# Optimization experiments

Hardware: AMD Instinct MI355X
Metric: run time of the kernel (lower is better)

The kernel has to match this reference:

```python
import jax, jax.numpy as jnp
import numpy as np

HEAD_DIM = 128
MAX_TIMESCALE = 10000.0
MIN_TIMESCALE = 1.0


def _rope(x, pos):
    # x: [B, S, H, D], pos: [B, S]
    d = x.shape[-1]
    fraction = 2.0 * jnp.arange(0, d // 2, dtype=jnp.float32) / d
    timescale = MIN_TIMESCALE * (MAX_TIMESCALE / MIN_TIMESCALE) ** fraction  # [D/2]
    sinusoid = pos.astype(jnp.float32)[..., None, None] / timescale  # [B,S,1,D/2]
    sin, cos = jnp.sin(sinusoid), jnp.cos(sinusoid)
    xf = x.astype(jnp.float32)
    x1, x2 = jnp.split(xf, 2, axis=-1)
    return jnp.concatenate((x1 * cos - x2 * sin, x2 * cos + x1 * sin), axis=-1).astype(x.dtype)


def setup_inputs() -> dict:
    key = jax.random.key(0)
    ks = jax.random.split(key, 5)
    B, T, D, N, K, H = 2, 2048, 2048, 16, 4, HEAD_DIM
    s = 0.02
    X = jax.random.normal(ks[0], (B, T, D), dtype=jnp.float32)
    q_positions = jnp.broadcast_to(jnp.arange(T, dtype=jnp.int32), (B, T))
    Wq = jax.random.normal(ks[1], (D, N, H), dtype=jnp.float32) * s
    Wk = jax.random.normal(ks[2], (D, K, H), dtype=jnp.float32) * s
    Wv = jax.random.normal(ks[3], (D, K, H), dtype=jnp.float32) * s
    Wo = jax.random.normal(ks[4], (N, H, D), dtype=jnp.float32) * s
    return {"X": X, "q_positions": q_positions, "Wq": Wq, "Wk": Wk, "Wv": Wv, "Wo": Wo}


def reference(X, q_positions, Wq, Wk, Wv, Wo):
    B, T, D = X.shape
    N, K = Wq.shape[1], Wk.shape[1]
    groups = N // K
    # fused QKV projections (DenseGeneral, no bias)
    q = jnp.einsum('btd,dnh->btnh', X, Wq)  # [B,T,N,H]
    k = jnp.einsum('btd,dkh->btkh', X, Wk)  # [B,T,K,H]
    v = jnp.einsum('btd,dkh->btkh', X, Wv)  # [B,T,K,H]
    # RoPE (note: original uses q_positions sin/cos for both q and k in the no-cache path)
    q = _rope(q, q_positions)
    k = _rope(k, q_positions)
    # GQA: broadcast kv heads to query heads
    k = jnp.repeat(k, groups, axis=2)  # [B,T,N,H]
    v = jnp.repeat(v, groups, axis=2)
    # attention with scale=1.0 and causal masking
    scores = jnp.einsum('btnh,bsnh->bnts', q, k)  # [B,N,T,T]
    causal = jnp.tril(jnp.ones((T, T), dtype=bool))
    scores = jnp.where(causal, scores, jnp.finfo(scores.dtype).min)
    probs = jax.nn.softmax(scores, axis=-1)
    attn = jnp.einsum('bnts,bsnh->btnh', probs, v)  # [B,T,N,H]
    # output projection contracting (head, head_dim)
    out = jnp.einsum('btnh,nhd->btd', attn, Wo)
    return out.astype(X.dtype)
```

## Files before the change

### kernel.cpp

```cpp
#include <hip/hip_runtime.h>
#include <math.h>

#define DEVI static __device__ __forceinline__

using f16x8 = __attribute__((ext_vector_type(8))) _Float16;
using h16x2 = __attribute__((ext_vector_type(2))) __fp16;
using f32x4  = __attribute__((ext_vector_type(4))) float;

constexpr int Bb = 2, Tt = 2048, Dd = 2048, NQ = 16, NK = 4, HD = 128;
constexpr int Mrows = Bb * Tt;
constexpr int QKVC  = NQ*HD + 2*NK*HD;
constexpr int KOFF  = NQ*HD;
constexpr int VOFF  = NQ*HD + NK*HD;

DEVI ushort f2h(float f) {
  _Float16 h = (_Float16)f;
  union { _Float16 h; ushort u; } v; v.h = h;
  return v.u;
}
DEVI float h2f(ushort u) {
  union { ushort u; _Float16 h; } v; v.u = u;
  return (float)v.h;
}

typedef const __attribute__((address_space(1))) unsigned* gp1;
typedef __attribute__((address_space(3))) unsigned* lp3;
DEVI void gload16(void* lds, const void* g) {
  __builtin_amdgcn_global_load_lds((gp1)g, (lp3)lds, 16, 0, 0);
}

__global__ void k_cvt(const float* __restrict__ x, ushort* __restrict__ o, int n4) {
  int i = blockIdx.x * blockDim.x + threadIdx.x;
  if (i >= n4) return;
  float4 v = ((const float4*)x)[i];
  ushort4 u;
  u.x = f2h(v.x); u.y = f2h(v.y); u.z = f2h(v.z); u.w = f2h(v.w);
  ((ushort4*)o)[i] = u;
}

__global__ void k_tconv(const float* __restrict__ in, ushort* __restrict__ out, int R, int C) {
  __shared__ float t[32][33];
  const int c0 = blockIdx.x * 32, r0 = blockIdx.y * 32;
  const int tx = threadIdx.x, ty = threadIdx.y;
#pragma unroll
  for (int i = 0; i < 32; i += 8)
    t[ty + i][tx] = in[(size_t)(r0 + ty + i) * C + (c0 + tx)];
  __syncthreads();
#pragma unroll
  for (int i = 0; i < 32; i += 8)
    out[(size_t)(c0 + ty + i) * R + (r0 + tx)] = f2h(t[tx][ty + i]);
}

DEVI void stv(float* p, float v)  { *p = v; }
DEVI void stv(ushort* p, float v) { *p = f2h(v); }

template <typename OT>
__launch_bounds__(256)
__global__ void k_gemm_bt(const ushort* __restrict__ A, const ushort* __restrict__ Bt,
                          OT* __restrict__ C, int M, int N, int Kd) {
  __shared__ char As[8192];
  __shared__ char Bs[8192];
  const int tid = threadIdx.x;
  const int l = tid & 63, w = tid >> 6;
  const int wr = w >> 1, wc = w & 1;
  const int lr = l & 15, lk = l >> 4;
  const size_t row0 = (size_t)blockIdx.y * 128, col0 = (size_t)blockIdx.x * 128;

  f32x4 acc[4][4];
#pragma unroll
  for (int i = 0; i < 4; ++i)
#pragma unroll
    for (int j = 0; j < 4; ++j) acc[i][j] = (f32x4){0.f, 0.f, 0.f, 0.f};

  const int c0i = tid, c1i = tid + 256;
  const int ra0 = c0i >> 2, sa0 = (c0i & 3) ^ ((ra0 >> 1) & 3);
  const int ra1 = c1i >> 2, sa1 = (c1i & 3) ^ ((ra1 >> 1) & 3);

  for (int kt = 0; kt < Kd; kt += 32) {
    if (kt) __syncthreads();
    gload16(As + c0i * 16, A + (row0 + ra0) * Kd + kt + sa0 * 8);
    gload16(As + c1i * 16, A + (row0 + ra1) * Kd + kt + sa1 * 8);
    gload16(Bs + c0i * 16, Bt + (col0 + ra0) * Kd + kt + sa0 * 8);
    gload16(Bs + c1i * 16, Bt + (col0 + ra1) * Kd + kt + sa1 * 8);
    __syncthreads();
    f16x8 af[4], bfr[4];
#pragma unroll
    for (int i = 0; i < 4; ++i) {
      int ra = wr * 64 + i * 16 + lr;
      af[i] = *(const f16x8*)(As + ra * 64 + ((lk ^ ((ra >> 1) & 3)) << 4));
      int rb = wc * 64 + i * 16 + lr;
      bfr[i] = *(const f16x8*)(Bs + rb * 64 + ((lk ^ ((rb >> 1) & 3)) << 4));
    }
#pragma unroll
    for (int i = 0; i < 4; ++i)
#pragma unroll
      for (int j = 0; j < 4; ++j)
        acc[i][j] = __builtin_amdgcn_mfma_f32_16x16x32_f16(af[i], bfr[j], acc[i][j], 0, 0, 0);
  }
#pragma unroll
  for (int i = 0; i < 4; ++i) {
    size_t r = row0 + wr * 64 + i * 16 + lk * 4;
#pragma unroll
    for (int j = 0; j < 4; ++j) {
      size_t cc = col0 + wc * 64 + j * 16 + lr;
#pragma unroll
      for (int rg = 0; rg < 4; ++rg) stv(&C[(r + rg) * N + cc], acc[i][j][rg]);
    }
  }
}

__global__ void k_rope_tab(const int* __restrict__ pos, float* __restrict__ tab) {
  int idx = blockIdx.x * blockDim.x + threadIdx.x;
  if (idx >= Mrows * 64) return;
  int m = idx >> 6, i = idx & 63;
  double a = (double)pos[m] * exp2(-0.20762050593045952 * (double)i);
  tab[idx * 2]     = (float)cos(a);
  tab[idx * 2 + 1] = (float)sin(a);
}

__global__ void k_rope(ushort* __restrict__ qkv, const float* __restrict__ tab) {
  int idx = blockIdx.x * blockDim.x + threadIdx.x;
  if (idx >= Mrows * 20 * 8) return;
  int chunk = idx & 7;
  int h20 = (idx >> 3) % 20;
  int m = idx / 160;
  int colbase = (h20 < 16) ? h20 * 128 : (KOFF + (h20 - 16) * 128);
  size_t base = (size_t)m * QKVC + colbase + chunk * 8;
  union { uint4 v; ushort s[8]; } A1, A2, O1, O2;
  A1.v = *(const uint4*)(qkv + base);
  A2.v = *(const uint4*)(qkv + base + 64);
  const float* tp = tab + ((size_t)m * 64 + chunk * 8) * 2;
#pragma unroll
  for (int j = 0; j < 8; ++j) {
    float c = tp[2 * j], s = tp[2 * j + 1];
    float x1 = h2f(A1.s[j]), x2 = h2f(A2.s[j]);
    O1.s[j] = f2h(x1 * c - x2 * s);
    O2.s[j] = f2h(x2 * c + x1 * s);
  }
  *(uint4*)(qkv + base) = O1.v;
  *(uint4*)(qkv + base + 64) = O2.v;
}

__global__ void k_vt(const ushort* __restrict__ qkv, ushort* __restrict__ vt) {
  __shared__ ushort t[32][33];
  const int bg = blockIdx.z, bq = bg >> 2, g = bg & 3;
  const int s0 = blockIdx.x * 32, h0 = blockIdx.y * 32;
  const int tx = threadIdx.x, ty = threadIdx.y;
#pragma unroll
  for (int i = 0; i < 32; i += 8)
    t[ty + i][tx] = qkv[(size_t)(bq * Tt + s0 + ty + i) * QKVC + VOFF + g * HD + h0 + tx];
  __syncthreads();
#pragma unroll
  for (int i = 0; i < 32; i += 8)
    vt[((size_t)bg * HD + h0 + ty + i) * Tt + (s0 + tx)] = t[tx][ty + i];
}

__launch_bounds__(512, 2)
__global__ void k_flash(const ushort* __restrict__ qkv, const ushort* __restrict__ vt,
                        ushort* __restrict__ attn) {
  __shared__ char Ks[2][16384];
  __shared__ char Vs[2][16384];
  __shared__ char Pl[8][2048];
  const int b = blockIdx.x;
  const int vv = b >> 8, u = b & 255;
  const int hid = u >> 3, p = u & 7;
  const int qt = vv ? p : (15 - p);
  const int bq = hid >> 4, n = hid & 15, g = n >> 2;
  const int tid = threadIdx.x, w = tid >> 6, l = tid & 63;
  const int lr = l & 15, lk = l >> 4;
  const int t0 = qt * 128;
  const int qrow = t0 + w * 16;
  const int qglob = qrow + lr;

  f16x8 qf[4];
  {
    const size_t qb = ((size_t)(bq * Tt + qrow + lr)) * QKVC + n * HD + lk * 8;
#pragma unroll
    for (int kt = 0; kt < 4; ++kt) qf[kt] = *(const f16x8*)(qkv + qb + kt * 32);
  }
  f32x4 O[8];
#pragma unroll
  for (int hb = 0; hb < 8; ++hb) O[hb] = (f32x4){0.f, 0.f, 0.f, 0.f};
  float m = -INFINITY, lsum = 0.f;

  const size_t kgbase = (size_t)(bq * Tt) * QKVC + KOFF + g * HD;
  const size_t vgbase = (size_t)(bq * 4 + g) * HD * Tt;
  const int ntiles = 2 * qt + 2;

  int srow[2], koin[2], hrow[2], voin[2];
#pragma unroll
  for (int cc = 0; cc < 2; ++cc) {
    int c = cc * 512 + tid;
    srow[cc] = c >> 4;
    koin[cc] = (((c & 15) << 4) ^ ((srow[cc] & 7) << 4)) >> 1;
    hrow[cc] = c >> 3;
    voin[cc] = (((c & 7) << 4) ^ ((hrow[cc] & 7) << 4)) >> 1;
  }

#define STAGE(buf, s0s)                                                              \
  {                                                                                  \
    _Pragma("unroll")                                                                \
    for (int cc = 0; cc < 2; ++cc) {                                                 \
      int c16 = (cc * 512 + tid) * 16;                                               \
      gload16(Ks[buf] + c16, qkv + kgbase + (size_t)((s0s) + srow[cc]) * QKVC + koin[cc]); \
      gload16(Vs[buf] + c16, vt + vgbase + (size_t)hrow[cc] * Tt + (s0s) + voin[cc]); \
    }                                                                                \
  }

  STAGE(0, 0);
  __syncthreads();

  for (int j = 0; j < ntiles; ++j) {
    const int cur = j & 1;
    if (j + 1 < ntiles) STAGE(cur ^ 1, (j + 1) * 64);
    const int s0 = j * 64;
    if (s0 <= qrow + 15) {
      f32x4 sc[4];
      __builtin_amdgcn_s_setprio(1);
#pragma unroll
      for (int ns = 0; ns < 4; ++ns) {
        f32x4 a = (f32x4){0.f, 0.f, 0.f, 0.f};
        int sl = ns * 16 + lr;
#pragma unroll
        for (int kt = 0; kt < 4; ++kt) {
          int inner = (kt * 64 + lk * 16) ^ ((sl & 7) << 4);
          f16x8 kf = *(const f16x8*)(Ks[cur] + sl * 256 + inner);
          a = __builtin_amdgcn_mfma_f32_16x16x32_f16(kf, qf[kt], a, 0, 0, 0);
        }
        sc[ns] = a;
      }
      __builtin_amdgcn_s_setprio(0);
      if (s0 + 63 > qrow) {
#pragma unroll
        for (int ns = 0; ns < 4; ++ns)
#pragma unroll
          for (int r = 0; r < 4; ++r)
            if (s0 + ns * 16 + lk * 4 + r > qglob) sc[ns][r] = -INFINITY;
      }
      float pm = -INFINITY;
#pragma unroll
      for (int ns = 0; ns < 4; ++ns)
        pm = fmaxf(pm, fmaxf(fmaxf(sc[ns][0], sc[ns][1]), fmaxf(sc[ns][2], sc[ns][3])));
      pm = fmaxf(pm, __shfl_xor(pm, 16));
      pm = fmaxf(pm, __shfl_xor(pm, 32));
      const bool doresc = !__all(pm - m <= 8.0f);
      float scl = 1.f;
      if (doresc) { float mn = fmaxf(m, pm); scl = __expf(m - mn); m = mn; }
      float rs = 0.f;
#pragma unroll
      for (int ns = 0; ns < 4; ++ns) {
#pragma unroll
        for (int r = 0; r < 4; ++r) sc[ns][r] = __expf(sc[ns][r] - m);
        rs += (sc[ns][0] + sc[ns][1]) + (sc[ns][2] + sc[ns][3]);
      }
      rs += __shfl_xor(rs, 16);
      rs += __shfl_xor(rs, 32);
      char* pwb = Pl[w] + lr * 128;
      const int swz = (lr & 7) << 4;
#pragma unroll
      for (int ns = 0; ns < 4; ++ns) {
        union { h16x2 h[2]; uint2 u; } pk;
        pk.h[0] = __builtin_amdgcn_cvt_pkrtz(sc[ns][0], sc[ns][1]);
        pk.h[1] = __builtin_amdgcn_cvt_pkrtz(sc[ns][2], sc[ns][3]);
        *(uint2*)(pwb + ((ns * 32 + lk * 8) ^ swz)) = pk.u;
      }
      if (doresc) {
        float sr[4];
#pragma unroll
        for (int r = 0; r < 4; ++r) sr[r] = __shfl(scl, lk * 4 + r);
#pragma unroll
        for (int hb = 0; hb < 8; ++hb)
#pragma unroll
          for (int r = 0; r < 4; ++r) O[hb][r] *= sr[r];
        lsum = lsum * scl + rs;
      } else {
        lsum += rs;
      }
      f16x8 pa0 = *(const f16x8*)(pwb + ((lk * 16) ^ swz));
      f16x8 pa1 = *(const f16x8*)(pwb + ((64 + lk * 16) ^ swz));
      __builtin_amdgcn_s_setprio(1);
#pragma unroll
      for (int hb = 0; hb < 8; ++hb) {
        int h = hb * 16 + lr;
        int inner0 = (lk * 16) ^ ((h & 7) << 4);
        f16x8 vf0 = *(const f16x8*)(Vs[cur] + h * 128 + inner0);
        O[hb] = __builtin_amdgcn_mfma_f32_16x16x32_f16(pa0, vf0, O[hb], 0, 0, 0);
        int inner1 = (64 + lk * 16) ^ ((h & 7) << 4);
        f16x8 vf1 = *(const f16x8*)(Vs[cur] + h * 128 + inner1);
        O[hb] = __builtin_amdgcn_mfma_f32_16x16x32_f16(pa1, vf1, O[hb], 0, 0, 0);
      }
      __builtin_amdgcn_s_setprio(0);
    }
    __syncthreads();
  }
#undef STAGE
  float iv[4];
#pragma unroll
  for (int r = 0; r < 4; ++r) iv[r] = 1.f / __shfl(lsum, lk * 4 + r);
#pragma unroll
  for (int hb = 0; hb < 8; ++hb)
#pragma unroll
    for (int r = 0; r < 4; ++r) {
      size_t orow = (size_t)(bq * Tt + qrow + lk * 4 + r);
      attn[orow * 2048 + n * HD + hb * 16 + lr] = f2h(O[hb][r] * iv[r]);
    }
}

extern "C" void kernel_launch(void* const* d_in, const int* in_sizes, int n_in,
                              void* d_out, int out_size, void* d_ws, size_t ws_size,
                              hipStream_t stream) {
  const float* X  = (const float*)d_in[0];
  const int*   qp = (const int*)d_in[1];
  const float* Wq = (const float*)d_in[2];
  const float* Wk = (const float*)d_in[3];
  const float* Wv = (const float*)d_in[4];
  const float* Wo = (const float*)d_in[5];
  float* out = (float*)d_out;
  char* ws = (char*)d_ws;

  ushort* Xf    = (ushort*)(ws + 0);
  ushort* WqkvT = (ushort*)(ws + 16777216);
  ushort* WoT   = (ushort*)(ws + 29360128);
  ushort* QKV   = (ushort*)(ws + 37748736);
  ushort* VT    = (ushort*)(ws + 62914560);
  ushort* attn  = (ushort*)(ws + 67108864);
  float*  tab   = (float*)(ws + 83886080);

  dim3 tb(32, 8);
  k_cvt<<<(Mrows * Dd / 4 + 255) / 256, 256, 0, stream>>>(X, Xf, Mrows * Dd / 4);
  k_tconv<<<dim3(64, 64), tb, 0, stream>>>(Wq, WqkvT, Dd, NQ * HD);
  k_tconv<<<dim3(16, 64), tb, 0, stream>>>(Wk, WqkvT + (size_t)KOFF * Dd, Dd, NK * HD);
  k_tconv<<<dim3(16, 64), tb, 0, stream>>>(Wv, WqkvT + (size_t)VOFF * Dd, Dd, NK * HD);
  k_tconv<<<dim3(64, 64), tb, 0, stream>>>(Wo, WoT, NQ * HD, Dd);
  k_gemm_bt<ushort><<<dim3(QKVC / 128, Mrows / 128), 256, 0, stream>>>(
      Xf, WqkvT, QKV, Mrows, QKVC, Dd);
  k_rope_tab<<<(Mrows * 64 + 255) / 256, 256, 0, stream>>>(qp, tab);
  k_rope<<<(Mrows * 160 + 255) / 256, 256, 0, stream>>>(QKV, tab);
  k_vt<<<dim3(Tt / 32, HD / 32, Bb * NK), tb, 0, stream>>>(QKV, VT);
  k_flash<<<dim3(512), 512, 0, stream>>>(QKV, VT, attn);
  k_gemm_bt<float><<<dim3(Dd / 128, Mrows / 128), 256, 0, stream>>>(
      attn, WoT, out, Mrows, Dd, Dd);
}
```

Measured before the change: 216.8 us.

## Switch flash attention to 32x32x16 MFMA with register-resident P and 4 waves

```diff
diff --git a/kernel.cpp b/kernel.cpp
--- a/kernel.cpp
+++ b/kernel.cpp
@@ -6,6 +6,7 @@
 using f16x8 = __attribute__((ext_vector_type(8))) _Float16;
 using h16x2 = __attribute__((ext_vector_type(2))) __fp16;
 using f32x4  = __attribute__((ext_vector_type(4))) float;
+using f32x16 = __attribute__((ext_vector_type(16))) float;
 
 constexpr int Bb = 2, Tt = 2048, Dd = 2048, NQ = 16, NK = 4, HD = 128;
 constexpr int Mrows = Bb * Tt;
@@ -150,61 +151,55 @@
   for (int i = 0; i < 32; i += 8)
     t[ty + i][tx] = qkv[(size_t)(bq * Tt + s0 + ty + i) * QKVC + VOFF + g * HD + h0 + tx];
   __syncthreads();
+  const int sx = (tx & 3) | ((tx & 8) >> 1) | ((tx & 4) << 1) | (tx & 16);
 #pragma unroll
   for (int i = 0; i < 32; i += 8)
-    vt[((size_t)bg * HD + h0 + ty + i) * Tt + (s0 + tx)] = t[tx][ty + i];
-}
-
-__launch_bounds__(512, 2)
+    vt[((size_t)bg * HD + h0 + ty + i) * Tt + (s0 + sx)] = t[tx][ty + i];
+}
+
+__launch_bounds__(256, 2)
 __global__ void k_flash(const ushort* __restrict__ qkv, const ushort* __restrict__ vt,
                         ushort* __restrict__ attn) {
   __shared__ char Ks[2][16384];
   __shared__ char Vs[2][16384];
-  __shared__ char Pl[8][2048];
   const int b = blockIdx.x;
   const int vv = b >> 8, u = b & 255;
   const int hid = u >> 3, p = u & 7;
   const int qt = vv ? p : (15 - p);
   const int bq = hid >> 4, n = hid & 15, g = n >> 2;
   const int tid = threadIdx.x, w = tid >> 6, l = tid & 63;
-  const int lr = l & 15, lk = l >> 4;
+  const int q5 = l & 31, hi = l >> 5;
   const int t0 = qt * 128;
-  const int qrow = t0 + w * 16;
-  const int qglob = qrow + lr;
-
-  f16x8 qf[4];
+  const int qrow = t0 + w * 32;
+  const int qglob = qrow + q5;
+
+  f16x8 qf[8];
   {
-    const size_t qb = ((size_t)(bq * Tt + qrow + lr)) * QKVC + n * HD + lk * 8;
-#pragma unroll
-    for (int kt = 0; kt < 4; ++kt) qf[kt] = *(const f16x8*)(qkv + qb + kt * 32);
-  }
-  f32x4 O[8];
-#pragma unroll
-  for (int hb = 0; hb < 8; ++hb) O[hb] = (f32x4){0.f, 0.f, 0.f, 0.f};
+    const size_t qb = ((size_t)(bq * Tt + qglob)) * QKVC + n * HD + hi * 8;
+#pragma unroll
+    for (int kc = 0; kc < 8; ++kc) qf[kc] = *(const f16x8*)(qkv + qb + kc * 16);
+  }
+  f32x16 O[4];
+#pragma unroll
+  for (int ht = 0; ht < 4; ++ht)
+#pragma unroll
+    for (int r = 0; r < 16; ++r) O[ht][r] = 0.f;
   float m = -INFINITY, lsum = 0.f;
 
   const size_t kgbase = (size_t)(bq * Tt) * QKVC + KOFF + g * HD;
   const size_t vgbase = (size_t)(bq * 4 + g) * HD * Tt;
   const int ntiles = 2 * qt + 2;
 
-  int srow[2], koin[2], hrow[2], voin[2];
-#pragma unroll
-  for (int cc = 0; cc < 2; ++cc) {
-    int c = cc * 512 + tid;
-    srow[cc] = c >> 4;
-    koin[cc] = (((c & 15) << 4) ^ ((srow[cc] & 7) << 4)) >> 1;
-    hrow[cc] = c >> 3;
-    voin[cc] = (((c & 7) << 4) ^ ((hrow[cc] & 7) << 4)) >> 1;
-  }
-
-#define STAGE(buf, s0s)                                                              \
-  {                                                                                  \
-    _Pragma("unroll")                                                                \
-    for (int cc = 0; cc < 2; ++cc) {                                                 \
-      int c16 = (cc * 512 + tid) * 16;                                               \
-      gload16(Ks[buf] + c16, qkv + kgbase + (size_t)((s0s) + srow[cc]) * QKVC + koin[cc]); \
-      gload16(Vs[buf] + c16, vt + vgbase + (size_t)hrow[cc] * Tt + (s0s) + voin[cc]); \
-    }                                                                                \
+#define STAGE(buf, s0s)                                                               \
+  {                                                                                   \
+    _Pragma("unroll")                                                                 \
+    for (int cc = 0; cc < 4; ++cc) {                                                  \
+      int c = cc * 256 + tid;                                                         \
+      int sK = c >> 4, gK = (c & 15) ^ (sK & 15);                                     \
+      gload16(Ks[buf] + c * 16, qkv + kgbase + (size_t)((s0s) + sK) * QKVC + gK * 8); \
+      int hV = c >> 3, gV = (c & 7) ^ (hV & 7);                                       \
+      gload16(Vs[buf] + c * 16, vt + vgbase + (size_t)hV * Tt + (s0s) + gV * 8);      \
+    }                                                                                 \
   }
 
   STAGE(0, 0);
@@ -214,95 +209,100 @@
     const int cur = j & 1;
     if (j + 1 < ntiles) STAGE(cur ^ 1, (j + 1) * 64);
     const int s0 = j * 64;
-    if (s0 <= qrow + 15) {
-      f32x4 sc[4];
+    if (s0 <= qrow + 31) {
+      f32x16 sc[2];
       __builtin_amdgcn_s_setprio(1);
 #pragma unroll
-      for (int ns = 0; ns < 4; ++ns) {
-        f32x4 a = (f32x4){0.f, 0.f, 0.f, 0.f};
-        int sl = ns * 16 + lr;
-#pragma unroll
-        for (int kt = 0; kt < 4; ++kt) {
-          int inner = (kt * 64 + lk * 16) ^ ((sl & 7) << 4);
-          f16x8 kf = *(const f16x8*)(Ks[cur] + sl * 256 + inner);
-          a = __builtin_amdgcn_mfma_f32_16x16x32_f16(kf, qf[kt], a, 0, 0, 0);
+      for (int st = 0; st < 2; ++st) {
+        f32x16 a;
+#pragma unroll
+        for (int r = 0; r < 16; ++r) a[r] = 0.f;
+        const int sl = st * 32 + q5;
+        const int ssw = (sl & 15) << 4;
+#pragma unroll
+        for (int kc = 0; kc < 8; ++kc) {
+          f16x8 kf = *(const f16x8*)(Ks[cur] + sl * 256 + (((kc * 32 + hi * 16)) ^ ssw));
+          a = __builtin_amdgcn_mfma_f32_32x32x16_f16(kf, qf[kc], a, 0, 0, 0);
         }
-        sc[ns] = a;
+        sc[st] = a;
       }
       __builtin_amdgcn_s_setprio(0);
       if (s0 + 63 > qrow) {
 #pragma unroll
-        for (int ns = 0; ns < 4; ++ns)
-#pragma unroll
-          for (int r = 0; r < 4; ++r)
-            if (s0 + ns * 16 + lk * 4 + r > qglob) sc[ns][r] = -INFINITY;
+        for (int st = 0; st < 2; ++st)
+#pragma unroll
+          for (int r = 0; r < 16; ++r) {
+            int sg = s0 + st * 32 + (r & 3) + 8 * (r >> 2) + 4 * hi;
+            if (sg > qglob) sc[st][r] = -INFINITY;
+          }
       }
       float pm = -INFINITY;
 #pragma unroll
-      for (int ns = 0; ns < 4; ++ns)
-        pm = fmaxf(pm, fmaxf(fmaxf(sc[ns][0], sc[ns][1]), fmaxf(sc[ns][2], sc[ns][3])));
-      pm = fmaxf(pm, __shfl_xor(pm, 16));
+      for (int st = 0; st < 2; ++st)
+#pragma unroll
+        for (int r = 0; r < 16; ++r) pm = fmaxf(pm, sc[st][r]);
       pm = fmaxf(pm, __shfl_xor(pm, 32));
       const bool doresc = !__all(pm - m <= 8.0f);
       float scl = 1.f;
       if (doresc) { float mn = fmaxf(m, pm); scl = __expf(m - mn); m = mn; }
       float rs = 0.f;
 #pragma unroll
-      for (int ns = 0; ns < 4; ++ns) {
-#pragma unroll
-        for (int r = 0; r < 4; ++r) sc[ns][r] = __expf(sc[ns][r] - m);
-        rs += (sc[ns][0] + sc[ns][1]) + (sc[ns][2] + sc[ns][3]);
-      }
-      rs += __shfl_xor(rs, 16);
+      for (int st = 0; st < 2; ++st)
+#pragma unroll
+        for (int r = 0; r < 16; ++r) { sc[st][r] = __expf(sc[st][r] - m); rs += sc[st][r]; }
       rs += __shfl_xor(rs, 32);
-      char* pwb = Pl[w] + lr * 128;
-      const int swz = (lr & 7) << 4;
-#pragma unroll
-      for (int ns = 0; ns < 4; ++ns) {
-        union { h16x2 h[2]; uint2 u; } pk;
-        pk.h[0] = __builtin_amdgcn_cvt_pkrtz(sc[ns][0], sc[ns][1]);
-        pk.h[1] = __builtin_amdgcn_cvt_pkrtz(sc[ns][2], sc[ns][3]);
-        *(uint2*)(pwb + ((ns * 32 + lk * 8) ^ swz)) = pk.u;
-      }
       if (doresc) {
-        float sr[4];
-#pragma unroll
-        for (int r = 0; r < 4; ++r) sr[r] = __shfl(scl, lk * 4 + r);
-#pragma unroll
-        for (int hb = 0; hb < 8; ++hb)
-#pragma unroll
-          for (int r = 0; r < 4; ++r) O[hb][r] *= sr[r];
+        float sr[16];
+#pragma unroll
+        for (int r = 0; r < 16; ++r) sr[r] = __shfl(scl, (r & 3) + 8 * (r >> 2) + 4 * hi);
+#pragma unroll
+        for (int ht = 0; ht < 4; ++ht)
+#pragma unroll
+          for (int r = 0; r < 16; ++r) O[ht][r] *= sr[r];
         lsum = lsum * scl + rs;
       } else {
         lsum += rs;
       }
-      f16x8 pa0 = *(const f16x8*)(pwb + ((lk * 16) ^ swz));
-      f16x8 pa1 = *(const f16x8*)(pwb + ((64 + lk * 16) ^ swz));
+      unsigned pw[2][8];
+#pragma unroll
+      for (int st = 0; st < 2; ++st)
+#pragma unroll
+        for (int i = 0; i < 8; ++i) {
+          union { h16x2 h; unsigned u; } t;
+          t.h = __builtin_amdgcn_cvt_pkrtz(sc[st][2 * i], sc[st][2 * i + 1]);
+          pw[st][i] = t.u;
+        }
       __builtin_amdgcn_s_setprio(1);
 #pragma unroll
-      for (int hb = 0; hb < 8; ++hb) {
-        int h = hb * 16 + lr;
-        int inner0 = (lk * 16) ^ ((h & 7) << 4);
-        f16x8 vf0 = *(const f16x8*)(Vs[cur] + h * 128 + inner0);
-        O[hb] = __builtin_amdgcn_mfma_f32_16x16x32_f16(pa0, vf0, O[hb], 0, 0, 0);
-        int inner1 = (64 + lk * 16) ^ ((h & 7) << 4);
-        f16x8 vf1 = *(const f16x8*)(Vs[cur] + h * 128 + inner1);
-        O[hb] = __builtin_amdgcn_mfma_f32_16x16x32_f16(pa1, vf1, O[hb], 0, 0, 0);
+      for (int ht = 0; ht < 4; ++ht) {
+        const int hrow = ht * 32 + q5;
+        const int hsw = (hrow & 7) << 4;
+#pragma unroll
+        for (int cc = 0; cc < 4; ++cc) {
+          const int st = cc >> 1, ch = cc & 1;
+          union { unsigned u[4]; f16x8 v; } pa;
+          pa.u[0] = pw[st][ch * 4 + 0];
+          pa.u[1] = pw[st][ch * 4 + 1];
+          pa.u[2] = pw[st][ch * 4 + 2];
+          pa.u[3] = pw[st][ch * 4 + 3];
+          f16x8 vf = *(const f16x8*)(Vs[cur] + hrow * 128 + (((cc * 2 + hi) << 4) ^ hsw));
+          O[ht] = __builtin_amdgcn_mfma_f32_32x32x16_f16(pa.v, vf, O[ht], 0, 0, 0);
+        }
       }
       __builtin_amdgcn_s_setprio(0);
     }
     __syncthreads();
   }
 #undef STAGE
-  float iv[4];
-#pragma unroll
-  for (int r = 0; r < 4; ++r) iv[r] = 1.f / __shfl(lsum, lk * 4 + r);
-#pragma unroll
-  for (int hb = 0; hb < 8; ++hb)
-#pragma unroll
-    for (int r = 0; r < 4; ++r) {
-      size_t orow = (size_t)(bq * Tt + qrow + lk * 4 + r);
-      attn[orow * 2048 + n * HD + hb * 16 + lr] = f2h(O[hb][r] * iv[r]);
+  float iv[16];
+#pragma unroll
+  for (int r = 0; r < 16; ++r) iv[r] = 1.f / __shfl(lsum, (r & 3) + 8 * (r >> 2) + 4 * hi);
+#pragma unroll
+  for (int ht = 0; ht < 4; ++ht)
+#pragma unroll
+    for (int r = 0; r < 16; ++r) {
+      size_t orow = (size_t)(bq * Tt + qrow + (r & 3) + 8 * (r >> 2) + 4 * hi);
+      attn[orow * 2048 + n * HD + ht * 32 + q5] = f2h(O[ht][r] * iv[r]);
     }
 }
 
@@ -337,7 +337,7 @@
   k_rope_tab<<<(Mrows * 64 + 255) / 256, 256, 0, stream>>>(qp, tab);
   k_rope<<<(Mrows * 160 + 255) / 256, 256, 0, stream>>>(QKV, tab);
   k_vt<<<dim3(Tt / 32, HD / 32, Bb * NK), tb, 0, stream>>>(QKV, VT);
-  k_flash<<<dim3(512), 512, 0, stream>>>(QKV, VT, attn);
+  k_flash<<<dim3(512), 256, 0, stream>>>(QKV, VT, attn);
   k_gemm_bt<float><<<dim3(Dd / 128, Mrows / 128), 256, 0, stream>>>(
       attn, WoT, out, Mrows, Dd, Dd);
 }
```

Measured after the change: 219.0 us. About the same (+1.0%).
